# Kernel optimization log

Hardware: AMD Instinct MI355X
Metric: run time of the kernel (lower is better)

## Reference

```python
import jax, jax.numpy as jnp
import numpy as np

TAF = 0.05
EPS = 1e-8  # matches torch CosineSimilarity default eps

def _normalize(x):
    # torch cosine sim divides by max(||x||, eps) per vector
    n = jnp.linalg.norm(x, axis=-1, keepdims=True)
    return x / jnp.maximum(n, EPS)

def setup_inputs() -> dict:
    key = jax.random.key(0)
    k1, k2, k3 = jax.random.split(key, 3)
    N, D = 8192, 128
    return {
        "z": jax.random.normal(k1, (N, D), dtype=jnp.float32),
        "z_p": jax.random.normal(k2, (N, D), dtype=jnp.float32),
        "z_n": jax.random.normal(k3, (N, D), dtype=jnp.float32),
    }

def reference(z, z_p, z_n):
    # Fused normalize + matmul instead of broadcasting [N, M, D] intermediates.
    zn = _normalize(z)
    p_sim = zn @ _normalize(z_p).T / TAF   # [N, M]
    n_sim = zn @ _normalize(z_n).T / TAF   # [N, K]
    logits = jnp.concatenate([p_sim, n_sim], axis=1)  # [N, M+K]
    labels = jnp.arange(logits.shape[0])
    logp = jax.nn.log_softmax(logits, axis=-1)
    loss = -jnp.mean(jnp.take_along_axis(logp, labels[:, None], axis=1))
    return loss
```

## Files before the change

### kernel.cpp

```cpp
#include <hip/hip_runtime.h>
#include <hip/hip_bf16.h>
#include <stdint.h>


#define TAF_F 0.05f
constexpr float LOG2E  = 1.4426950408889634f;
constexpr float SCALE  = LOG2E / TAF_F;
constexpr float OFFSET = -20.0f * LOG2E;

constexpr int N_ROWS     = 8192;
constexpr int D_DIM      = 128;
constexpr int TWO_N      = 16384;
constexpr int NJ         = 16;
constexpr int JCHUNK     = TWO_N / NJ;
constexpr int BN_TILE    = 64;
constexpr int BLOCK_ROWS = 256;
constexpr int WAVE_ROWS  = 64;

typedef __bf16 bf16x8 __attribute__((ext_vector_type(8)));
typedef float  f32x4  __attribute__((ext_vector_type(4)));

#if __has_builtin(__builtin_amdgcn_exp2f)
#define EXP2(x) __builtin_amdgcn_exp2f(x)
#else
#define EXP2(x) exp2f(x)
#endif

__global__ void normalize_diag_kernel(const float* __restrict__ z,
                                      const float* __restrict__ zp,
                                      const float* __restrict__ znm,
                                      __bf16* __restrict__ znb,
                                      __bf16* __restrict__ bnb,
                                      float* __restrict__ diag) {
    const int i    = blockIdx.x;
    const int t    = threadIdx.x;
    const int lane = t & 63;
    const int wv   = t >> 6;

    const float vz = z[i * D_DIM + t];
    const float vp = zp[i * D_DIM + t];
    const float vn = znm[i * D_DIM + t];

    float sz = vz * vz, sp = vp * vp, sn = vn * vn, szp = vz * vp;
#pragma unroll
    for (int o = 32; o >= 1; o >>= 1) {
        sz  += __shfl_xor(sz, o);
        sp  += __shfl_xor(sp, o);
        sn  += __shfl_xor(sn, o);
        szp += __shfl_xor(szp, o);
    }
    __shared__ float red[2][4];
    if (lane == 0) { red[wv][0] = sz; red[wv][1] = sp; red[wv][2] = sn; red[wv][3] = szp; }
    __syncthreads();
    sz  = red[0][0] + red[1][0];
    sp  = red[0][1] + red[1][1];
    sn  = red[0][2] + red[1][2];
    szp = red[0][3] + red[1][3];

    const float rz = 1.0f / fmaxf(sqrtf(sz), 1e-8f);
    const float rp = 1.0f / fmaxf(sqrtf(sp), 1e-8f);
    const float rn = 1.0f / fmaxf(sqrtf(sn), 1e-8f);

    znb[i * D_DIM + t]            = (__bf16)(vz * rz);
    bnb[i * D_DIM + t]            = (__bf16)(vp * rp);
    bnb[(N_ROWS + i) * D_DIM + t] = (__bf16)(vn * rn);
    if (t == 0) diag[i] = szp * rz * rp * (1.0f / TAF_F);
}

__global__ __launch_bounds__(256, 2) void partial_lse_kernel(
        const __bf16* __restrict__ znb,
        const __bf16* __restrict__ bnb,
        float* __restrict__ partial) {
    __shared__ __align__(16) unsigned char lds[BN_TILE * D_DIM * 2];

    const int tid  = threadIdx.x;
    const int lane = tid & 63;
    const int wv   = tid >> 6;
    const int l15  = lane & 15;
    const int l4   = lane >> 4;
    const int rowBase = blockIdx.x * BLOCK_ROWS + wv * WAVE_ROWS;
    const int jBase   = blockIdx.y * JCHUNK;

    bf16x8 a[4][4];
#pragma unroll
    for (int s = 0; s < 4; ++s)
#pragma unroll
        for (int kk = 0; kk < 4; ++kk) {
            const __bf16* p = znb + (size_t)(rowBase + s * 16 + l15) * D_DIM + kk * 32 + l4 * 8;
            a[s][kk] = *reinterpret_cast<const bf16x8*>(p);
        }

    float sums[4][4];
#pragma unroll
    for (int s = 0; s < 4; ++s)
#pragma unroll
        for (int e = 0; e < 4; ++e) sums[s][e] = 0.0f;

    const unsigned char* srcBase = reinterpret_cast<const unsigned char*>(bnb);

    for (int jt = 0; jt < JCHUNK / BN_TILE; ++jt) {
        const int j0 = jBase + jt * BN_TILE;
        const unsigned char* src = srcBase + (size_t)j0 * 256;
#pragma unroll
        for (int it = 0; it < 4; ++it) {
            const int c  = it * 256 + tid;
            const uint4 v = *reinterpret_cast<const uint4*>(src + c * 16);
            const int cd = c ^ ((c >> 4) & 7);
            *reinterpret_cast<uint4*>(lds + cd * 16) = v;
        }
        __syncthreads();

#pragma unroll
        for (int jsub = 0; jsub < 4; ++jsub) {
            bf16x8 b[4];
            const int r = jsub * 16 + l15;
#pragma unroll
            for (int kk = 0; kk < 4; ++kk) {
                const int cl = r * 16 + kk * 4 + l4;
                const int ca = cl ^ (r & 7);
                b[kk] = *reinterpret_cast<const bf16x8*>(lds + ca * 16);
            }
#pragma unroll
            for (int s = 0; s < 4; ++s) {
                f32x4 acc = {0.0f, 0.0f, 0.0f, 0.0f};
#pragma unroll
                for (int kk = 0; kk < 4; ++kk)
                    acc = __builtin_amdgcn_mfma_f32_16x16x32_bf16(a[s][kk], b[kk], acc, 0, 0, 0);
#pragma unroll
                for (int e = 0; e < 4; ++e)
                    sums[s][e] += EXP2(fmaf(acc[e], SCALE, OFFSET));
            }
        }
        __syncthreads();
    }

#pragma unroll
    for (int s = 0; s < 4; ++s)
#pragma unroll
        for (int e = 0; e < 4; ++e) {
            float v = sums[s][e];
            v += __shfl_xor(v, 1);
            v += __shfl_xor(v, 2);
            v += __shfl_xor(v, 4);
            v += __shfl_xor(v, 8);
            sums[s][e] = v;
        }
    if (l15 == 0) {
#pragma unroll
        for (int s = 0; s < 4; ++s)
#pragma unroll
            for (int e = 0; e < 4; ++e) {
                const int row = rowBase + s * 16 + l4 * 4 + e;
                partial[(size_t)row * NJ + blockIdx.y] = sums[s][e];
            }
    }
}

__global__ void finalize_rows_kernel(const float* __restrict__ partial,
                                     const float* __restrict__ diag,
                                     float* __restrict__ blocksum) {
    const int t = threadIdx.x;
    const int r = blockIdx.x * 256 + t;
    float se = 0.0f;
#pragma unroll
    for (int c = 0; c < NJ; ++c) se += partial[(size_t)r * NJ + c];
    float res = 20.0f + logf(se) - diag[r];
#pragma unroll
    for (int o = 32; o >= 1; o >>= 1) res += __shfl_xor(res, o);
    __shared__ float red[4];
    if ((t & 63) == 0) red[t >> 6] = res;
    __syncthreads();
    if (t == 0) blocksum[blockIdx.x] = red[0] + red[1] + red[2] + red[3];
}

__global__ void final_kernel(const float* __restrict__ blocksum,
                             float* __restrict__ out) {
    const int t = threadIdx.x;
    float v = (t < 32) ? blocksum[t] : 0.0f;
#pragma unroll
    for (int o = 32; o >= 1; o >>= 1) v += __shfl_xor(v, o);
    if (t == 0) out[0] = v * (1.0f / (float)N_ROWS);
}

extern "C" void kernel_launch(void* const* d_in, const int* in_sizes, int n_in,
                              void* d_out, int out_size, void* d_ws, size_t ws_size,
                              hipStream_t stream) {
    const float* z   = (const float*)d_in[0];
    const float* zp  = (const float*)d_in[1];
    const float* znm = (const float*)d_in[2];

    char* ws = (char*)d_ws;
    __bf16* znb     = (__bf16*)(ws);
    __bf16* bnb     = (__bf16*)(ws + 2097152);
    float*  diag    = (float*)(ws + 6291456);
    float*  partial = (float*)(ws + 6324224);
    float*  blocksum= (float*)(ws + 6848512);
    float*  out     = (float*)d_out;

    normalize_diag_kernel<<<N_ROWS, 128, 0, stream>>>(z, zp, znm, znb, bnb, diag);
    partial_lse_kernel<<<dim3(N_ROWS / BLOCK_ROWS, NJ), 256, 0, stream>>>(znb, bnb, partial);
    finalize_rows_kernel<<<N_ROWS / 256, 256, 0, stream>>>(partial, diag, blocksum);
    final_kernel<<<1, 64, 0, stream>>>(blocksum, out);
}
```

Measured before the change: 51.41 us.

## Double-buffer LDS tiles, double column splits, and use one wave per normalize row

The partial LSE kernel now double-buffers the B tile in LDS. It prefetches the next tile into registers while computing the current one, then writes it to the other buffer, which removes one barrier per iteration. The column split NJ goes from 16 to 32 and launch bounds rise to 4 blocks per CU, giving 1024 blocks to fill the GPU better at the cost of more partial sums and register pressure. The normalize kernel handles one row per wave with float2 loads and no LDS reduction, and the workspace offset is adjusted for the larger partial buffer.

```diff
diff --git a/kernel.cpp b/kernel.cpp
--- a/kernel.cpp
+++ b/kernel.cpp
@@ -11,13 +11,16 @@
 constexpr int N_ROWS     = 8192;
 constexpr int D_DIM      = 128;
 constexpr int TWO_N      = 16384;
-constexpr int NJ         = 16;
+constexpr int NJ         = 32;
 constexpr int JCHUNK     = TWO_N / NJ;
 constexpr int BN_TILE    = 64;
+constexpr int NT         = JCHUNK / BN_TILE;
 constexpr int BLOCK_ROWS = 256;
 constexpr int WAVE_ROWS  = 64;
+constexpr int TILE_BYTES = BN_TILE * D_DIM * 2;
 
 typedef __bf16 bf16x8 __attribute__((ext_vector_type(8)));
+typedef __bf16 bf16x2 __attribute__((ext_vector_type(2)));
 typedef float  f32x4  __attribute__((ext_vector_type(4)));
 
 #if __has_builtin(__builtin_amdgcn_exp2f)
@@ -32,16 +35,18 @@
                                       __bf16* __restrict__ znb,
                                       __bf16* __restrict__ bnb,
                                       float* __restrict__ diag) {
-    const int i    = blockIdx.x;
-    const int t    = threadIdx.x;
-    const int lane = t & 63;
-    const int wv   = t >> 6;
-
-    const float vz = z[i * D_DIM + t];
-    const float vp = zp[i * D_DIM + t];
-    const float vn = znm[i * D_DIM + t];
-
-    float sz = vz * vz, sp = vp * vp, sn = vn * vn, szp = vz * vp;
+    const int wv   = threadIdx.x >> 6;
+    const int lane = threadIdx.x & 63;
+    const int i    = blockIdx.x * 4 + wv;
+
+    const float2 vz = *reinterpret_cast<const float2*>(z   + (size_t)i * D_DIM + lane * 2);
+    const float2 vp = *reinterpret_cast<const float2*>(zp  + (size_t)i * D_DIM + lane * 2);
+    const float2 vn = *reinterpret_cast<const float2*>(znm + (size_t)i * D_DIM + lane * 2);
+
+    float sz  = vz.x * vz.x + vz.y * vz.y;
+    float sp  = vp.x * vp.x + vp.y * vp.y;
+    float sn  = vn.x * vn.x + vn.y * vn.y;
+    float szp = vz.x * vp.x + vz.y * vp.y;
 #pragma unroll
     for (int o = 32; o >= 1; o >>= 1) {
         sz  += __shfl_xor(sz, o);
@@ -49,29 +54,24 @@
         sn  += __shfl_xor(sn, o);
         szp += __shfl_xor(szp, o);
     }
-    __shared__ float red[2][4];
-    if (lane == 0) { red[wv][0] = sz; red[wv][1] = sp; red[wv][2] = sn; red[wv][3] = szp; }
-    __syncthreads();
-    sz  = red[0][0] + red[1][0];
-    sp  = red[0][1] + red[1][1];
-    sn  = red[0][2] + red[1][2];
-    szp = red[0][3] + red[1][3];
-
     const float rz = 1.0f / fmaxf(sqrtf(sz), 1e-8f);
     const float rp = 1.0f / fmaxf(sqrtf(sp), 1e-8f);
     const float rn = 1.0f / fmaxf(sqrtf(sn), 1e-8f);
 
-    znb[i * D_DIM + t]            = (__bf16)(vz * rz);
-    bnb[i * D_DIM + t]            = (__bf16)(vp * rp);
-    bnb[(N_ROWS + i) * D_DIM + t] = (__bf16)(vn * rn);
-    if (t == 0) diag[i] = szp * rz * rp * (1.0f / TAF_F);
-}
-
-__global__ __launch_bounds__(256, 2) void partial_lse_kernel(
+    bf16x2 oz = { (__bf16)(vz.x * rz), (__bf16)(vz.y * rz) };
+    bf16x2 op = { (__bf16)(vp.x * rp), (__bf16)(vp.y * rp) };
+    bf16x2 on = { (__bf16)(vn.x * rn), (__bf16)(vn.y * rn) };
+    *reinterpret_cast<bf16x2*>(znb + (size_t)i * D_DIM + lane * 2)            = oz;
+    *reinterpret_cast<bf16x2*>(bnb + (size_t)i * D_DIM + lane * 2)            = op;
+    *reinterpret_cast<bf16x2*>(bnb + (size_t)(N_ROWS + i) * D_DIM + lane * 2) = on;
+    if (lane == 0) diag[i] = szp * rz * rp * (1.0f / TAF_F);
+}
+
+__global__ __launch_bounds__(256, 4) void partial_lse_kernel(
         const __bf16* __restrict__ znb,
         const __bf16* __restrict__ bnb,
         float* __restrict__ partial) {
-    __shared__ __align__(16) unsigned char lds[BN_TILE * D_DIM * 2];
+    __shared__ __align__(16) unsigned char lds[TILE_BYTES * 2];
 
     const int tid  = threadIdx.x;
     const int lane = tid & 63;
@@ -98,18 +98,30 @@
 
     const unsigned char* srcBase = reinterpret_cast<const unsigned char*>(bnb);
 
-    for (int jt = 0; jt < JCHUNK / BN_TILE; ++jt) {
-        const int j0 = jBase + jt * BN_TILE;
-        const unsigned char* src = srcBase + (size_t)j0 * 256;
+    {
+        const unsigned char* src = srcBase + (size_t)jBase * 256;
 #pragma unroll
         for (int it = 0; it < 4; ++it) {
             const int c  = it * 256 + tid;
-            const uint4 v = *reinterpret_cast<const uint4*>(src + c * 16);
             const int cd = c ^ ((c >> 4) & 7);
-            *reinterpret_cast<uint4*>(lds + cd * 16) = v;
-        }
+            *reinterpret_cast<uint4*>(lds + cd * 16) =
+                *reinterpret_cast<const uint4*>(src + (size_t)c * 16);
+        }
+    }
+
+    for (int jt = 0; jt < NT; ++jt) {
         __syncthreads();
 
+        const bool havenext = (jt + 1 < NT);
+        uint4 vstage[4];
+        if (havenext) {
+            const unsigned char* src = srcBase + (size_t)(jBase + (jt + 1) * BN_TILE) * 256;
+#pragma unroll
+            for (int it = 0; it < 4; ++it)
+                vstage[it] = *reinterpret_cast<const uint4*>(src + (size_t)(it * 256 + tid) * 16);
+        }
+
+        const unsigned char* ldsr = lds + (jt & 1) * TILE_BYTES;
 #pragma unroll
         for (int jsub = 0; jsub < 4; ++jsub) {
             bf16x8 b[4];
@@ -118,7 +130,7 @@
             for (int kk = 0; kk < 4; ++kk) {
                 const int cl = r * 16 + kk * 4 + l4;
                 const int ca = cl ^ (r & 7);
-                b[kk] = *reinterpret_cast<const bf16x8*>(lds + ca * 16);
+                b[kk] = *reinterpret_cast<const bf16x8*>(ldsr + ca * 16);
             }
 #pragma unroll
             for (int s = 0; s < 4; ++s) {
@@ -131,7 +143,16 @@
                     sums[s][e] += EXP2(fmaf(acc[e], SCALE, OFFSET));
             }
         }
-        __syncthreads();
+
+        if (havenext) {
+            unsigned char* ldsw = lds + ((jt + 1) & 1) * TILE_BYTES;
+#pragma unroll
+            for (int it = 0; it < 4; ++it) {
+                const int c  = it * 256 + tid;
+                const int cd = c ^ ((c >> 4) & 7);
+                *reinterpret_cast<uint4*>(ldsw + cd * 16) = vstage[it];
+            }
+        }
     }
 
 #pragma unroll
@@ -194,10 +215,10 @@
     __bf16* bnb     = (__bf16*)(ws + 2097152);
     float*  diag    = (float*)(ws + 6291456);
     float*  partial = (float*)(ws + 6324224);
-    float*  blocksum= (float*)(ws + 6848512);
+    float*  blocksum= (float*)(ws + 7372800);
     float*  out     = (float*)d_out;
 
-    normalize_diag_kernel<<<N_ROWS, 128, 0, stream>>>(z, zp, znm, znb, bnb, diag);
+    normalize_diag_kernel<<<N_ROWS / 4, 256, 0, stream>>>(z, zp, znm, znb, bnb, diag);
     partial_lse_kernel<<<dim3(N_ROWS / BLOCK_ROWS, NJ), 256, 0, stream>>>(znb, bnb, partial);
     finalize_rows_kernel<<<N_ROWS / 256, 256, 0, stream>>>(partial, diag, blocksum);
     final_kernel<<<1, 64, 0, stream>>>(blocksum, out);
```

New measurement: 166.0 us. 3.23x slower.
